# Kernel optimization log

Measured on AMD Instinct MI355X. Metric: run time of the kernel, lower is better.

Reference implementation:

```python
import jax, jax.numpy as jnp
import numpy as np

B, L, H = 32, 2048, 1024


def setup_inputs() -> dict:
    key = jax.random.key(0)
    k1, k2, k3, k4, k5 = jax.random.split(key, 5)
    stdv = 1.0 / np.sqrt(H)
    return {
        "hidden": jax.random.normal(k1, (B, H), dtype=jnp.float32),
        "encoder_outputs": jax.random.normal(k2, (L, B, H), dtype=jnp.float32),
        "attn_w": jax.random.normal(k3, (H, 2 * H), dtype=jnp.float32) * stdv,
        "attn_b": jax.random.normal(k4, (H,), dtype=jnp.float32) * stdv,
        "v": jax.random.normal(k5, (H,), dtype=jnp.float32) * stdv,
    }


def reference(hidden, encoder_outputs, attn_w, attn_b, v):
    # encoder_outputs: [L, B, H] -> batch-first [B, L, H]
    enc = jnp.transpose(encoder_outputs, (1, 0, 2))
    # Additive (Bahdanau) energies. Split the concat-linear into two GEMMs to
    # avoid materializing the [B, L, 2H] concat:
    #   attn([H_rep, enc]) = hidden @ W_h^T + enc @ W_e^T + b
    w_h, w_e = attn_w[:, :H], attn_w[:, H:]  # each [H, 2H]->[H, H]
    proj = (jnp.einsum("bh,oh->bo", hidden, w_h)[:, None, :]
            + jnp.einsum("blh,oh->blo", enc, w_e)
            + attn_b)
    energy = jnp.tanh(proj)                   # [B, L, H]
    scores = jnp.einsum("blh,h->bl", energy, v)  # [B, L]
    attn = jax.nn.softmax(scores, axis=-1)       # [B, L]
    context = jnp.einsum("bl,blh->bh", attn, enc)  # [B, H]
    return context[None, :, :]  # [1, B, H] matching context.transpose(0,1)
```

## Files before the change

kernel.cpp:

```cpp
#include <hip/hip_runtime.h>
#include <hip/hip_bf16.h>
#include <math.h>

#define Hdim 1024
#define Bdim 32
#define Ldim 2048
#define Mtot (Bdim*Ldim)

typedef __attribute__((ext_vector_type(8))) short short8v;
typedef __attribute__((ext_vector_type(4))) short short4v;
typedef __attribute__((ext_vector_type(4))) float floatx4;

static __device__ inline short f2bf(float f) {
    union { float f; unsigned u; } x; x.f = f;
    unsigned r = x.u + 0x7FFF + ((x.u >> 16) & 1);
    return (short)(r >> 16);
}
static __device__ inline float bf2f(short s) {
    union { unsigned u; float f; } x; x.u = ((unsigned)(unsigned short)s) << 16;
    return x.f;
}

static __device__ inline float fast_tanh(float x) {
    float t = 2.0f * x;
    t = fminf(fmaxf(t, -30.0f), 30.0f);
    float e = __expf(t);
    return (e - 1.0f) / (e + 1.0f);
}

typedef __attribute__((address_space(1))) const void GVT;
typedef __attribute__((address_space(3))) void LVT;
static __device__ inline void gload_lds16(const void* g, void* l) {
    __builtin_amdgcn_global_load_lds((GVT*)g, (LVT*)l, 16, 0, 0);
}

__global__ __launch_bounds__(256) void convert_enc_kernel(
    const float* __restrict__ enc, short* __restrict__ enc_bf)
{
    size_t i = ((size_t)blockIdx.x * 256 + threadIdx.x) * 8;
    float4 a = *(const float4*)(enc + i);
    float4 b = *(const float4*)(enc + i + 4);
    short8v o;
    o[0]=f2bf(a.x); o[1]=f2bf(a.y); o[2]=f2bf(a.z); o[3]=f2bf(a.w);
    o[4]=f2bf(b.x); o[5]=f2bf(b.y); o[6]=f2bf(b.z); o[7]=f2bf(b.w);
    *(short8v*)(enc_bf + i) = o;
}

__global__ __launch_bounds__(256) void convert_w_kernel(
    const float* __restrict__ attn_w, short* __restrict__ w_bf)
{
    int t = blockIdx.x * 256 + threadIdx.x;
    int o = t >> 7;
    int c = t & 127;
    const float* src = attn_w + (size_t)o * 2 * Hdim + Hdim + c * 8;
    float4 a = *(const float4*)(src);
    float4 b = *(const float4*)(src + 4);
    short8v v;
    v[0]=f2bf(a.x); v[1]=f2bf(a.y); v[2]=f2bf(a.z); v[3]=f2bf(a.w);
    v[4]=f2bf(b.x); v[5]=f2bf(b.y); v[6]=f2bf(b.z); v[7]=f2bf(b.w);
    *(short8v*)(w_bf + (size_t)o * Hdim + c * 8) = v;
}

__global__ __launch_bounds__(256) void qproj_kernel(
    const float* __restrict__ hidden, const float* __restrict__ attn_w,
    const float* __restrict__ attn_b, float* __restrict__ qbuf)
{
    int w = blockIdx.x * 4 + (threadIdx.x >> 6);
    int lane = threadIdx.x & 63;
    int o = w >> 5;
    int b = w & 31;
    const float* hrow = hidden + b * Hdim;
    const float* wrow = attn_w + (size_t)o * 2 * Hdim;
    float s = 0.f;
    #pragma unroll
    for (int i = 0; i < 16; i++) s += hrow[lane + i*64] * wrow[lane + i*64];
    s += __shfl_xor(s, 1);  s += __shfl_xor(s, 2);  s += __shfl_xor(s, 4);
    s += __shfl_xor(s, 8);  s += __shfl_xor(s, 16); s += __shfl_xor(s, 32);
    if (lane == 0) qbuf[b * Hdim + o] = s + attn_b[o];
}

#define BM 128
#define BN 128
#define BK 32

__global__ __launch_bounds__(256) void scores_kernel(
    const short* __restrict__ enc_bf,
    const short* __restrict__ w_bf,
    const float* __restrict__ qbuf,
    const float* __restrict__ vvec,
    float* __restrict__ spart)
{
    __shared__ short As[BM * BK];
    __shared__ short Bs[BN * BK];
    __shared__ float sred[BM][2];

    int bx    = blockIdx.x;
    int nblk  = bx & 7;
    int mtile = bx >> 3;
    int m0 = mtile * BM;
    int n0 = nblk * BN;

    int tid  = threadIdx.x;
    int w    = tid >> 6;
    int l    = tid & 63;
    int wr = w >> 1, wc = w & 1;
    int r15 = l & 15;
    int kc  = l >> 4;

    int subrow = l >> 2;
    int chunk  = l & 3;
    const short* ag0 = enc_bf + (size_t)(m0 + w*32 + subrow) * Hdim + chunk * 8;
    const short* ag1 = ag0 + (size_t)16 * Hdim;
    const short* bg0 = w_bf  + (size_t)(n0 + w*32 + subrow) * Hdim + chunk * 8;
    const short* bg1 = bg0 + (size_t)16 * Hdim;
    short* al0 = As + (w*32) * BK;
    short* al1 = As + (w*32 + 16) * BK;
    short* bl0 = Bs + (w*32) * BK;
    short* bl1 = Bs + (w*32 + 16) * BK;

    int aoff[4], boff[4];
    #pragma unroll
    for (int i = 0; i < 4; i++) {
        aoff[i] = (wr*64 + i*16 + r15) * BK + kc * 8;
        boff[i] = (wc*64 + i*16 + r15) * BK + kc * 8;
    }

    floatx4 acc[4][4];
    #pragma unroll
    for (int i = 0; i < 4; i++)
        #pragma unroll
        for (int j = 0; j < 4; j++) acc[i][j] = (floatx4){0.f, 0.f, 0.f, 0.f};

    for (int kt = 0; kt < Hdim / BK; kt++) {
        __syncthreads();
        gload_lds16(ag0, al0);
        gload_lds16(ag1, al1);
        gload_lds16(bg0, bl0);
        gload_lds16(bg1, bl1);
        ag0 += BK; ag1 += BK; bg0 += BK; bg1 += BK;
        __syncthreads();

        short8v af[4], bf[4];
        #pragma unroll
        for (int mi = 0; mi < 4; mi++) af[mi] = *(const short8v*)(&As[aoff[mi]]);
        #pragma unroll
        for (int ni = 0; ni < 4; ni++) bf[ni] = *(const short8v*)(&Bs[boff[ni]]);
        #pragma unroll
        for (int mi = 0; mi < 4; mi++)
            #pragma unroll
            for (int ni = 0; ni < 4; ni++)
                acc[mi][ni] = __builtin_amdgcn_mfma_f32_16x16x32_bf16(af[mi], bf[ni], acc[mi][ni], 0, 0, 0);
    }

    int rg = l >> 4;
    #pragma unroll
    for (int mi = 0; mi < 4; mi++) {
        float rs[4] = {0.f, 0.f, 0.f, 0.f};
        #pragma unroll
        for (int ni = 0; ni < 4; ni++) {
            int o = n0 + wc*64 + ni*16 + r15;
            float vo = vvec[o];
            #pragma unroll
            for (int reg = 0; reg < 4; reg++) {
                int trow = wr*64 + mi*16 + rg*4 + reg;
                int b = trow & 31;
                float p = acc[mi][ni][reg] + qbuf[b * Hdim + o];
                rs[reg] += fast_tanh(p) * vo;
            }
        }
        #pragma unroll
        for (int reg = 0; reg < 4; reg++) {
            float s = rs[reg];
            s += __shfl_xor(s, 1); s += __shfl_xor(s, 2);
            s += __shfl_xor(s, 4); s += __shfl_xor(s, 8);
            if (r15 == 0) {
                int trow = wr*64 + mi*16 + rg*4 + reg;
                sred[trow][wc] = s;
            }
        }
    }
    __syncthreads();
    if (tid < BM)
        spart[(size_t)nblk * Mtot + m0 + tid] = sred[tid][0] + sred[tid][1];
}

__global__ __launch_bounds__(256) void softmax_kernel(
    const float* __restrict__ spart, float* __restrict__ attn)
{
    int b = blockIdx.x;
    int t = threadIdx.x;
    __shared__ float rmax[4], rsum[4];
    float sv[8];
    float mx = -1e30f;
    #pragma unroll
    for (int i = 0; i < 8; i++) {
        int l = t + i * 256;
        int m = l * Bdim + b;
        float s = 0.f;
        #pragma unroll
        for (int p = 0; p < 8; p++) s += spart[(size_t)p * Mtot + m];
        sv[i] = s;
        mx = fmaxf(mx, s);
    }
    #pragma unroll
    for (int off = 1; off < 64; off <<= 1) mx = fmaxf(mx, __shfl_xor(mx, off));
    if ((t & 63) == 0) rmax[t >> 6] = mx;
    __syncthreads();
    mx = fmaxf(fmaxf(rmax[0], rmax[1]), fmaxf(rmax[2], rmax[3]));
    float sum = 0.f;
    #pragma unroll
    for (int i = 0; i < 8; i++) { sv[i] = __expf(sv[i] - mx); sum += sv[i]; }
    #pragma unroll
    for (int off = 1; off < 64; off <<= 1) sum += __shfl_xor(sum, off);
    if ((t & 63) == 0) rsum[t >> 6] = sum;
    __syncthreads();
    sum = rsum[0] + rsum[1] + rsum[2] + rsum[3];
    float inv = 1.f / sum;
    #pragma unroll
    for (int i = 0; i < 8; i++)
        attn[(size_t)b * Ldim + t + i * 256] = sv[i] * inv;
}

__global__ __launch_bounds__(256) void context_part_kernel(
    const short* __restrict__ enc_bf,
    const float* __restrict__ attn,
    float* __restrict__ cpart)
{
    int b = blockIdx.x & 31;
    int c = blockIdx.x >> 5;
    int t = threadIdx.x;
    float a0 = 0.f, a1 = 0.f, a2 = 0.f, a3 = 0.f;
    int l0 = c * 32;
    for (int i = 0; i < 32; i++) {
        int l = l0 + i;
        float a = attn[(size_t)b * Ldim + l];
        short4v e = *(const short4v*)(enc_bf + (size_t)(l * Bdim + b) * Hdim + t * 4);
        a0 += a * bf2f(e.x); a1 += a * bf2f(e.y);
        a2 += a * bf2f(e.z); a3 += a * bf2f(e.w);
    }
    float4 r; r.x = a0; r.y = a1; r.z = a2; r.w = a3;
    *(float4*)(cpart + ((size_t)c * Bdim + b) * Hdim + t * 4) = r;
}

__global__ __launch_bounds__(256) void context_reduce_kernel(
    const float* __restrict__ cpart, float* __restrict__ out)
{
    int idx = blockIdx.x * 256 + threadIdx.x;
    float s = 0.f;
    for (int c = 0; c < 64; c++) s += cpart[(size_t)c * (Bdim * Hdim) + idx];
    out[idx] = s;
}

extern "C" void kernel_launch(void* const* d_in, const int* in_sizes, int n_in,
                              void* d_out, int out_size, void* d_ws, size_t ws_size,
                              hipStream_t stream)
{
    const float* hidden = (const float*)d_in[0];
    const float* enc    = (const float*)d_in[1];
    const float* attn_w = (const float*)d_in[2];
    const float* attn_b = (const float*)d_in[3];
    const float* vvec   = (const float*)d_in[4];
    float* out = (float*)d_out;

    char* ws = (char*)d_ws;
    size_t off = 0;
    short* enc_bf = (short*)(ws + off); off += (size_t)Mtot * Hdim * 2;
    short* w_bf   = (short*)(ws + off); off += (size_t)Hdim * Hdim * 2;
    float* qbuf   = (float*)(ws + off); off += (size_t)Bdim * Hdim * 4;
    float* spart  = (float*)(ws + off); off += (size_t)8 * Mtot * 4;
    float* attnp  = (float*)(ws + off); off += (size_t)Mtot * 4;
    float* cpart  = (float*)(ws + off);

    convert_enc_kernel<<<32768, 256, 0, stream>>>(enc, enc_bf);
    convert_w_kernel<<<512, 256, 0, stream>>>(attn_w, w_bf);
    qproj_kernel<<<8192, 256, 0, stream>>>(hidden, attn_w, attn_b, qbuf);
    scores_kernel<<<4096, 256, 0, stream>>>(enc_bf, w_bf, qbuf, vvec, spart);
    softmax_kernel<<<Bdim, 256, 0, stream>>>(spart, attnp);
    context_part_kernel<<<2048, 256, 0, stream>>>(enc_bf, attnp, cpart);
    context_reduce_kernel<<<128, 256, 0, stream>>>(cpart, out);
}
```

Baseline: 351.9 us.

## Double-buffer LDS tiles in scores GEMM and remap blocks per XCD

Adds a two-stage LDS ping-pong so the global-to-LDS loads for the next K tile are issued before the MFMA work on the current tile, with one barrier per iteration instead of two. Block indices are remapped so that each XCD handles a contiguous range of M tiles across all N blocks, which is meant to improve L2 reuse of encoder rows. Launch bounds now request 4 blocks per CU. Doubling LDS per block and the occupancy hint may limit registers or residency.

```diff
diff --git a/kernel.cpp b/kernel.cpp
--- a/kernel.cpp
+++ b/kernel.cpp
@@ -83,20 +83,22 @@
 #define BN 128
 #define BK 32
 
-__global__ __launch_bounds__(256) void scores_kernel(
+__global__ __launch_bounds__(256, 4) void scores_kernel(
     const short* __restrict__ enc_bf,
     const short* __restrict__ w_bf,
     const float* __restrict__ qbuf,
     const float* __restrict__ vvec,
     float* __restrict__ spart)
 {
-    __shared__ short As[BM * BK];
-    __shared__ short Bs[BN * BK];
+    __shared__ short As[2][BM * BK];
+    __shared__ short Bs[2][BN * BK];
     __shared__ float sred[BM][2];
 
-    int bx    = blockIdx.x;
-    int nblk  = bx & 7;
-    int mtile = bx >> 3;
+    int hw = blockIdx.x;
+    int xcd = hw & 7;
+    int i5  = hw >> 3;
+    int nblk  = i5 & 7;
+    int mtile = xcd * 64 + (i5 >> 3);
     int m0 = mtile * BM;
     int n0 = nblk * BN;
 
@@ -113,10 +115,8 @@
     const short* ag1 = ag0 + (size_t)16 * Hdim;
     const short* bg0 = w_bf  + (size_t)(n0 + w*32 + subrow) * Hdim + chunk * 8;
     const short* bg1 = bg0 + (size_t)16 * Hdim;
-    short* al0 = As + (w*32) * BK;
-    short* al1 = As + (w*32 + 16) * BK;
-    short* bl0 = Bs + (w*32) * BK;
-    short* bl1 = Bs + (w*32 + 16) * BK;
+    int al0 = (w*32) * BK;
+    int al1 = (w*32 + 16) * BK;
 
     int aoff[4], boff[4];
     #pragma unroll
@@ -131,25 +131,35 @@
         #pragma unroll
         for (int j = 0; j < 4; j++) acc[i][j] = (floatx4){0.f, 0.f, 0.f, 0.f};
 
+    gload_lds16(ag0, &As[0][al0]);
+    gload_lds16(ag1, &As[0][al1]);
+    gload_lds16(bg0, &Bs[0][al0]);
+    gload_lds16(bg1, &Bs[0][al1]);
+    ag0 += BK; ag1 += BK; bg0 += BK; bg1 += BK;
+    __syncthreads();
+
+    #pragma unroll 2
     for (int kt = 0; kt < Hdim / BK; kt++) {
-        __syncthreads();
-        gload_lds16(ag0, al0);
-        gload_lds16(ag1, al1);
-        gload_lds16(bg0, bl0);
-        gload_lds16(bg1, bl1);
-        ag0 += BK; ag1 += BK; bg0 += BK; bg1 += BK;
-        __syncthreads();
-
+        int cur = kt & 1;
+        if (kt < Hdim / BK - 1) {
+            int nxt = cur ^ 1;
+            gload_lds16(ag0, &As[nxt][al0]);
+            gload_lds16(ag1, &As[nxt][al1]);
+            gload_lds16(bg0, &Bs[nxt][al0]);
+            gload_lds16(bg1, &Bs[nxt][al1]);
+            ag0 += BK; ag1 += BK; bg0 += BK; bg1 += BK;
+        }
         short8v af[4], bf[4];
         #pragma unroll
-        for (int mi = 0; mi < 4; mi++) af[mi] = *(const short8v*)(&As[aoff[mi]]);
-        #pragma unroll
-        for (int ni = 0; ni < 4; ni++) bf[ni] = *(const short8v*)(&Bs[boff[ni]]);
+        for (int mi = 0; mi < 4; mi++) af[mi] = *(const short8v*)(&As[cur][aoff[mi]]);
+        #pragma unroll
+        for (int ni = 0; ni < 4; ni++) bf[ni] = *(const short8v*)(&Bs[cur][boff[ni]]);
         #pragma unroll
         for (int mi = 0; mi < 4; mi++)
             #pragma unroll
             for (int ni = 0; ni < 4; ni++)
                 acc[mi][ni] = __builtin_amdgcn_mfma_f32_16x16x32_bf16(af[mi], bf[ni], acc[mi][ni], 0, 0, 0);
+        __syncthreads();
     }
 
     int rg = l >> 4;
```

New measurement: 306.7 us. 12.8% less time.

## Rewrite scores GEMM with 256x256 tiles, double-buffered LDS and XCD-aware mapping

Applied to the files above, without the earlier changes.

Reworks the bf16 scores GEMM to use 256x256x64 tiles with 512 threads, a double-buffered LDS pipeline, XOR-swizzled LDS layout, interleaved staging of the next K tile between MFMA phases, and s_setprio around MFMA blocks. Block indices are remapped so tiles sharing M rows land on the same XCD for L2 reuse. Partial score buffers shrink from 8 to 4 N-splits, and softmax now sums 4 partials. The larger tile raises arithmetic intensity and hides global loads, at the cost of one block per CU and heavy register use.

```diff
diff --git a/kernel.cpp b/kernel.cpp
--- a/kernel.cpp
+++ b/kernel.cpp
@@ -79,82 +79,143 @@
     if (lane == 0) qbuf[b * Hdim + o] = s + attn_b[o];
 }
 
-#define BM 128
-#define BN 128
-#define BK 32
-
-__global__ __launch_bounds__(256) void scores_kernel(
+#define NKT 16
+
+__global__ __launch_bounds__(512, 1) void scores_kernel(
     const short* __restrict__ enc_bf,
     const short* __restrict__ w_bf,
     const float* __restrict__ qbuf,
     const float* __restrict__ vvec,
     float* __restrict__ spart)
 {
-    __shared__ short As[BM * BK];
-    __shared__ short Bs[BN * BK];
-    __shared__ float sred[BM][2];
-
-    int bx    = blockIdx.x;
-    int nblk  = bx & 7;
-    int mtile = bx >> 3;
-    int m0 = mtile * BM;
-    int n0 = nblk * BN;
-
-    int tid  = threadIdx.x;
-    int w    = tid >> 6;
-    int l    = tid & 63;
-    int wr = w >> 1, wc = w & 1;
+    __shared__ short As[2][256*64];
+    __shared__ short Bs[2][256*64];
+    __shared__ float sred[256][4];
+
+    int hw  = blockIdx.x;
+    int xcd = hw & 7;
+    int i7  = hw >> 3;
+    int nblk  = i7 & 3;
+    int mtile = xcd * 32 + (i7 >> 2);
+    int m0 = mtile * 256;
+    int n0 = nblk * 256;
+
+    int tid = threadIdx.x;
+    int w   = tid >> 6;
+    int l   = tid & 63;
+    int wr  = w >> 2;
+    int wc  = w & 3;
     int r15 = l & 15;
     int kc  = l >> 4;
-
-    int subrow = l >> 2;
-    int chunk  = l & 3;
-    const short* ag0 = enc_bf + (size_t)(m0 + w*32 + subrow) * Hdim + chunk * 8;
-    const short* ag1 = ag0 + (size_t)16 * Hdim;
-    const short* bg0 = w_bf  + (size_t)(n0 + w*32 + subrow) * Hdim + chunk * 8;
-    const short* bg1 = bg0 + (size_t)16 * Hdim;
-    short* al0 = As + (w*32) * BK;
-    short* al1 = As + (w*32 + 16) * BK;
-    short* bl0 = Bs + (w*32) * BK;
-    short* bl1 = Bs + (w*32 + 16) * BK;
-
-    int aoff[4], boff[4];
-    #pragma unroll
-    for (int i = 0; i < 4; i++) {
-        aoff[i] = (wr*64 + i*16 + r15) * BK + kc * 8;
-        boff[i] = (wc*64 + i*16 + r15) * BK + kc * 8;
+    int rg  = l >> 4;
+
+    const int glsw = (l >> 3) * Hdim + (((l & 7) ^ (l >> 3)) * 8);
+
+#define STAGE_A(h, bb, k0) do { \
+    const short* _g = enc_bf + (size_t)(m0 + (h)*128 + w*16) * Hdim + (k0) + glsw; \
+    gload_lds16(_g,            &As[bb][(h)*8192 + w*1024]);        \
+    gload_lds16(_g + 8*Hdim,   &As[bb][(h)*8192 + w*1024 + 512]);  \
+} while (0)
+#define STAGE_B(h, bb, k0) do { \
+    const short* _g = w_bf + (size_t)(n0 + (h)*128 + w*16) * Hdim + (k0) + glsw; \
+    gload_lds16(_g,            &Bs[bb][(h)*8192 + w*1024]);        \
+    gload_lds16(_g + 8*Hdim,   &Bs[bb][(h)*8192 + w*1024 + 512]);  \
+} while (0)
+#define LDA(mi, kk) (*(const short8v*)(&As[cur][(wr*128 + (mi)*16 + r15)*64 + ((((kk)*4 + kc) ^ (l & 7)) * 8)]))
+#define LDB(ni, kk) (*(const short8v*)(&Bs[cur][(wc*64  + (ni)*16 + r15)*64 + ((((kk)*4 + kc) ^ (l & 7)) * 8)]))
+
+    floatx4 acc[8][4];
+    #pragma unroll
+    for (int i = 0; i < 8; i++)
+        #pragma unroll
+        for (int j = 0; j < 4; j++) acc[i][j] = (floatx4){0.f, 0.f, 0.f, 0.f};
+
+    short8v af[4][2], bf[4][2];
+
+    STAGE_A(0, 0, 0); STAGE_A(1, 0, 0);
+    STAGE_B(0, 0, 0); STAGE_B(1, 0, 0);
+
+    for (int kt = 0; kt < NKT; kt++) {
+        int cur = kt & 1;
+        int nxt = cur ^ 1;
+        int kn  = (kt + 1) * 64;
+
+        if (kt < NKT - 1) {
+            STAGE_A(0, nxt, kn);
+            asm volatile("s_waitcnt vmcnt(2)" ::: "memory");
+        } else {
+            asm volatile("s_waitcnt vmcnt(0)" ::: "memory");
+        }
+        __builtin_amdgcn_s_barrier();
+        #pragma unroll
+        for (int mi = 0; mi < 4; mi++)
+            #pragma unroll
+            for (int kk = 0; kk < 2; kk++) af[mi][kk] = LDA(mi, kk);
+        #pragma unroll
+        for (int ni = 0; ni < 2; ni++)
+            #pragma unroll
+            for (int kk = 0; kk < 2; kk++) bf[ni][kk] = LDB(ni, kk);
+        __builtin_amdgcn_s_setprio(1);
+        #pragma unroll
+        for (int mi = 0; mi < 4; mi++)
+            #pragma unroll
+            for (int ni = 0; ni < 2; ni++)
+                #pragma unroll
+                for (int kk = 0; kk < 2; kk++)
+                    acc[mi][ni] = __builtin_amdgcn_mfma_f32_16x16x32_bf16(af[mi][kk], bf[ni][kk], acc[mi][ni], 0, 0, 0);
+        __builtin_amdgcn_s_setprio(0);
+        __builtin_amdgcn_s_barrier();
+
+        #pragma unroll
+        for (int ni = 2; ni < 4; ni++)
+            #pragma unroll
+            for (int kk = 0; kk < 2; kk++) bf[ni][kk] = LDB(ni, kk);
+        if (kt < NKT - 1) STAGE_A(1, nxt, kn);
+        __builtin_amdgcn_s_barrier();
+        __builtin_amdgcn_s_setprio(1);
+        #pragma unroll
+        for (int mi = 0; mi < 4; mi++)
+            #pragma unroll
+            for (int ni = 2; ni < 4; ni++)
+                #pragma unroll
+                for (int kk = 0; kk < 2; kk++)
+                    acc[mi][ni] = __builtin_amdgcn_mfma_f32_16x16x32_bf16(af[mi][kk], bf[ni][kk], acc[mi][ni], 0, 0, 0);
+        __builtin_amdgcn_s_setprio(0);
+        __builtin_amdgcn_s_barrier();
+
+        #pragma unroll
+        for (int mi = 0; mi < 4; mi++)
+            #pragma unroll
+            for (int kk = 0; kk < 2; kk++) af[mi][kk] = LDA(mi + 4, kk);
+        if (kt < NKT - 1) STAGE_B(0, nxt, kn);
+        __builtin_amdgcn_s_barrier();
+        __builtin_amdgcn_s_setprio(1);
+        #pragma unroll
+        for (int mi = 0; mi < 4; mi++)
+            #pragma unroll
+            for (int ni = 0; ni < 2; ni++)
+                #pragma unroll
+                for (int kk = 0; kk < 2; kk++)
+                    acc[mi + 4][ni] = __builtin_amdgcn_mfma_f32_16x16x32_bf16(af[mi][kk], bf[ni][kk], acc[mi + 4][ni], 0, 0, 0);
+        __builtin_amdgcn_s_setprio(0);
+        __builtin_amdgcn_s_barrier();
+
+        if (kt < NKT - 1) STAGE_B(1, nxt, kn);
+        __builtin_amdgcn_s_barrier();
+        __builtin_amdgcn_s_setprio(1);
+        #pragma unroll
+        for (int mi = 0; mi < 4; mi++)
+            #pragma unroll
+            for (int ni = 2; ni < 4; ni++)
+                #pragma unroll
+                for (int kk = 0; kk < 2; kk++)
+                    acc[mi + 4][ni] = __builtin_amdgcn_mfma_f32_16x16x32_bf16(af[mi][kk], bf[ni][kk], acc[mi + 4][ni], 0, 0, 0);
+        __builtin_amdgcn_s_setprio(0);
+        __builtin_amdgcn_s_barrier();
     }
 
-    floatx4 acc[4][4];
-    #pragma unroll
-    for (int i = 0; i < 4; i++)
-        #pragma unroll
-        for (int j = 0; j < 4; j++) acc[i][j] = (floatx4){0.f, 0.f, 0.f, 0.f};
-
-    for (int kt = 0; kt < Hdim / BK; kt++) {
-        __syncthreads();
-        gload_lds16(ag0, al0);
-        gload_lds16(ag1, al1);
-        gload_lds16(bg0, bl0);
-        gload_lds16(bg1, bl1);
-        ag0 += BK; ag1 += BK; bg0 += BK; bg1 += BK;
-        __syncthreads();
-
-        short8v af[4], bf[4];
-        #pragma unroll
-        for (int mi = 0; mi < 4; mi++) af[mi] = *(const short8v*)(&As[aoff[mi]]);
-        #pragma unroll
-        for (int ni = 0; ni < 4; ni++) bf[ni] = *(const short8v*)(&Bs[boff[ni]]);
-        #pragma unroll
-        for (int mi = 0; mi < 4; mi++)
-            #pragma unroll
-            for (int ni = 0; ni < 4; ni++)
-                acc[mi][ni] = __builtin_amdgcn_mfma_f32_16x16x32_bf16(af[mi], bf[ni], acc[mi][ni], 0, 0, 0);
-    }
-
-    int rg = l >> 4;
-    #pragma unroll
-    for (int mi = 0; mi < 4; mi++) {
+    #pragma unroll
+    for (int mi = 0; mi < 8; mi++) {
         float rs[4] = {0.f, 0.f, 0.f, 0.f};
         #pragma unroll
         for (int ni = 0; ni < 4; ni++) {
@@ -162,9 +223,8 @@
             float vo = vvec[o];
             #pragma unroll
             for (int reg = 0; reg < 4; reg++) {
-                int trow = wr*64 + mi*16 + rg*4 + reg;
-                int b = trow & 31;
-                float p = acc[mi][ni][reg] + qbuf[b * Hdim + o];
+                int r = wr*128 + mi*16 + rg*4 + reg;
+                float p = acc[mi][ni][reg] + qbuf[(r & 31) * Hdim + o];
                 rs[reg] += fast_tanh(p) * vo;
             }
         }
@@ -174,18 +234,23 @@
             s += __shfl_xor(s, 1); s += __shfl_xor(s, 2);
             s += __shfl_xor(s, 4); s += __shfl_xor(s, 8);
             if (r15 == 0) {
-                int trow = wr*64 + mi*16 + rg*4 + reg;
-                sred[trow][wc] = s;
+                int r = wr*128 + mi*16 + rg*4 + reg;
+                sred[r][wc] = s;
             }
         }
     }
     __syncthreads();
-    if (tid < BM)
-        spart[(size_t)nblk * Mtot + m0 + tid] = sred[tid][0] + sred[tid][1];
+    if (tid < 256)
+        spart[(size_t)nblk * Mtot + m0 + tid] = sred[tid][0] + sred[tid][1] + sred[tid][2] + sred[tid][3];
+#undef STAGE_A
+#undef STAGE_B
+#undef LDA
+#undef LDB
 }
 
 __global__ __launch_bounds__(256) void softmax_kernel(
-    const float* __restrict__ spart, float* __restrict__ attn)
+    const float* __restrict__ spart,
+    float* __restrict__ attn)
 {
     int b = blockIdx.x;
     int t = threadIdx.x;
@@ -198,7 +263,7 @@
         int m = l * Bdim + b;
         float s = 0.f;
         #pragma unroll
-        for (int p = 0; p < 8; p++) s += spart[(size_t)p * Mtot + m];
+        for (int p = 0; p < 4; p++) s += spart[(size_t)p * Mtot + m];
         sv[i] = s;
         mx = fmaxf(mx, s);
     }
@@ -267,14 +332,14 @@
     short* enc_bf = (short*)(ws + off); off += (size_t)Mtot * Hdim * 2;
     short* w_bf   = (short*)(ws + off); off += (size_t)Hdim * Hdim * 2;
     float* qbuf   = (float*)(ws + off); off += (size_t)Bdim * Hdim * 4;
-    float* spart  = (float*)(ws + off); off += (size_t)8 * Mtot * 4;
+    float* spart  = (float*)(ws + off); off += (size_t)4 * Mtot * 4;
     float* attnp  = (float*)(ws + off); off += (size_t)Mtot * 4;
     float* cpart  = (float*)(ws + off);
 
     convert_enc_kernel<<<32768, 256, 0, stream>>>(enc, enc_bf);
     convert_w_kernel<<<512, 256, 0, stream>>>(attn_w, w_bf);
     qproj_kernel<<<8192, 256, 0, stream>>>(hidden, attn_w, attn_b, qbuf);
-    scores_kernel<<<4096, 256, 0, stream>>>(enc_bf, w_bf, qbuf, vvec, spart);
+    scores_kernel<<<1024, 512, 0, stream>>>(enc_bf, w_bf, qbuf, vvec, spart);
     softmax_kernel<<<Bdim, 256, 0, stream>>>(spart, attnp);
     context_part_kernel<<<2048, 256, 0, stream>>>(enc_bf, attnp, cpart);
     context_reduce_kernel<<<128, 256, 0, stream>>>(cpart, out);
```

Result: faster. 312.9 us (-11.1%).
